# Kernel optimization log

Measured on AMD Instinct MI355X. Metric: run time of the kernel, lower is better.

The kernel has to match this reference:

```python
import jax, jax.numpy as jnp
import numpy as np

EPS = 1e-5

def _conv3x3(x, w, stride=1):
    # x: [N,C,H,W], w: [O,C,3,3]
    return jax.lax.conv_general_dilated(
        x, w, window_strides=(stride, stride), padding=((1, 1), (1, 1)),
        dimension_numbers=('NCHW', 'OIHW', 'NCHW'))

def _bn(x, gamma, beta, mean, var):
    # eval-mode BatchNorm2d over channel axis 1
    inv = jax.lax.rsqrt(var + EPS)
    return (x - mean[None, :, None, None]) * (gamma * inv)[None, :, None, None] + beta[None, :, None, None]

def setup_inputs() -> dict:
    key = jax.random.key(0)
    ks = jax.random.split(key, 8)
    C = 128
    x = jax.random.normal(ks[0], (64, C, 56, 56), dtype=jnp.float32)
    w1 = jax.random.normal(ks[1], (C, C, 3, 3), dtype=jnp.float32) * 0.05
    w2 = jax.random.normal(ks[2], (C, C, 3, 3), dtype=jnp.float32) * 0.05
    gamma1 = jnp.ones((C,), jnp.float32)
    beta1 = jnp.zeros((C,), jnp.float32)
    mean1 = jax.random.normal(ks[3], (C,), dtype=jnp.float32) * 0.1
    var1 = jax.random.uniform(ks[4], (C,), minval=0.5, maxval=1.5, dtype=jnp.float32)
    gamma2 = jnp.ones((C,), jnp.float32)
    beta2 = jnp.zeros((C,), jnp.float32)
    mean2 = jax.random.normal(ks[5], (C,), dtype=jnp.float32) * 0.1
    var2 = jax.random.uniform(ks[6], (C,), minval=0.5, maxval=1.5, dtype=jnp.float32)
    return {"x": x, "w1": w1, "w2": w2,
            "gamma1": gamma1, "beta1": beta1, "mean1": mean1, "var1": var1,
            "gamma2": gamma2, "beta2": beta2, "mean2": mean2, "var2": var2}

def reference(x, w1, w2, gamma1, beta1, mean1, var1, gamma2, beta2, mean2, var2):
    # BasicBlock forward. The voting loop over global dict d is a no-op (d = {}).
    residual = x
    out = _conv3x3(x, w1, stride=1)
    out = jax.nn.relu(_bn(out, gamma1, beta1, mean1, var1))
    out = _conv3x3(out, w2, stride=1)
    out = _bn(out, gamma2, beta2, mean2, var2)
    return jax.nn.relu(out + residual)
```

## Files before the change

### kernel.cpp

```cpp
#include <hip/hip_runtime.h>
#include <cstdint>

typedef __attribute__((ext_vector_type(8))) short bf16x8;
typedef __attribute__((ext_vector_type(4))) float f32x4;
typedef unsigned short u16;
typedef uint32_t u32;

#define HW56 56
#define HWSQ 3136
#define MTOT 200704
#define CCH 128
#define BM 128
#define NSTEP 18
#define NBLK (MTOT / BM)
#define NB_PER_XCD (NBLK / 8)

__device__ __forceinline__ u16 f2bf(float f) {
  u32 u = __builtin_bit_cast(u32, f);
  u = (u + 0x7fffu + ((u >> 16) & 1u)) >> 16;
  return (u16)u;
}
__device__ __forceinline__ float bf2f(u16 h) {
  return __builtin_bit_cast(float, (u32)h << 16);
}
__device__ __forceinline__ void gload16(const void* g, void* l) {
  __builtin_amdgcn_global_load_lds((const __attribute__((address_space(1))) void*)g,
                                   (__attribute__((address_space(3))) void*)l, 16, 0, 0);
}

__global__ __launch_bounds__(256) void pack_x_kernel(const float* __restrict__ x,
                                                     u16* __restrict__ xb) {
  __shared__ u16 t[128 * 65];
  const int tid = threadIdx.x;
  const int lane = tid & 63, wv = tid >> 6;
  const int p0 = blockIdx.x * 64;
  const int n = p0 / HWSQ, hw0 = p0 % HWSQ;
  const float* src = x + (size_t)(n * CCH) * HWSQ + hw0;
#pragma unroll
  for (int k = 0; k < 32; ++k) {
    const int c = wv * 32 + k;
    t[c * 65 + lane] = f2bf(src[(size_t)c * HWSQ + lane]);
  }
  __syncthreads();
  u16* dst = xb + (size_t)p0 * CCH;
#pragma unroll
  for (int it = 0; it < 4; ++it) {
    const int u = it * 256 + tid;
    const int pos = u >> 4, ch0 = (u & 15) * 8;
    u32 vv[4];
#pragma unroll
    for (int q = 0; q < 4; ++q) {
      const u16 a = t[(ch0 + 2 * q) * 65 + pos];
      const u16 b = t[(ch0 + 2 * q + 1) * 65 + pos];
      vv[q] = (u32)a | ((u32)b << 16);
    }
    uint4 v; v.x = vv[0]; v.y = vv[1]; v.z = vv[2]; v.w = vv[3];
    *(uint4*)(dst + (size_t)pos * CCH + ch0) = v;
  }
}

__global__ __launch_bounds__(256) void pack_w_kernel(
    const float* __restrict__ w1, const float* __restrict__ w2,
    const float* __restrict__ g1, const float* __restrict__ be1,
    const float* __restrict__ mu1, const float* __restrict__ va1,
    const float* __restrict__ g2, const float* __restrict__ be2,
    const float* __restrict__ mu2, const float* __restrict__ va2,
    u16* __restrict__ w1p, u16* __restrict__ w2p,
    float* __restrict__ b1, float* __restrict__ b2, float* __restrict__ zp) {
  const int idx = blockIdx.x * 256 + threadIdx.x;
  if (idx < 2 * 147456) {
    const int which = idx >= 147456;
    const int j = which ? idx - 147456 : idx;
    const int t = j >> 14;
    const int oc = (j >> 7) & 127;
    const int ic = j & 127;
    const float* w = which ? w2 : w1;
    const float* gg = which ? g2 : g1;
    const float* va = which ? va2 : va1;
    const float s = gg[oc] * rsqrtf(va[oc] + 1e-5f);
    const float val = w[(size_t)(oc * 128 + ic) * 9 + t] * s;
    (which ? w2p : w1p)[j] = f2bf(val);
  }
  if (blockIdx.x == 0) {
    const int t = threadIdx.x;
    if (t < 128) {
      const float s1 = g1[t] * rsqrtf(va1[t] + 1e-5f);
      b1[t] = be1[t] - mu1[t] * s1;
      const float s2 = g2[t] * rsqrtf(va2[t] + 1e-5f);
      b2[t] = be2[t] - mu2[t] * s2;
    }
    if (t < 64) zp[t] = 0.f;
  }
}

template <int PASS>
__global__ __launch_bounds__(256, 2) void conv_mfma(
    const u16* __restrict__ src, const u16* __restrict__ wp,
    const float* __restrict__ bias, const u16* __restrict__ resid,
    u16* __restrict__ outb, float* __restrict__ outf,
    const char* __restrict__ zp) {
  __shared__ __align__(1024) char lds[65536];
  const int tid = threadIdx.x;
  const int wave = tid >> 6, lane = tid & 63;
  const int bid = blockIdx.x;
  const int swz = (bid & 7) * NB_PER_XCD + (bid >> 3);
  const int m0 = swz * BM;
  const int wm = wave >> 1, wn = wave & 1;

  const int g = lane & 7;
  int ah[4], aw[4];
  long long aoff[4], boff[4];
#pragma unroll
  for (int i = 0; i < 4; ++i) {
    const int r = wave * 32 + i * 8 + (lane >> 3);
    const int pos = m0 + r;
    const int hw = pos % HWSQ;
    ah[i] = hw / HW56;
    aw[i] = hw % HW56;
    const int gsw = g ^ (r & 7);
    aoff[i] = (long long)pos * 256 + gsw * 16;
    boff[i] = (long long)r * 256 + gsw * 16;
  }
  const char* srcb = (const char*)src;
  const char* wpb = (const char*)wp;

  auto stage = [&](int buf, int s) {
    const int t = s >> 1, kh = s & 1;
    const int dyo = t / 3 - 1, dxo = t % 3 - 1;
    const long long adelta = (long long)(dyo * HW56 + dxo) * 256 + kh * 128;
    const long long bdelta = (long long)t * 32768 + kh * 128;
    char* ldsA = lds + buf * 16384;
    char* ldsB = lds + 32768 + buf * 16384;
#pragma unroll
    for (int i = 0; i < 4; ++i) {
      const int hh = ah[i] + dyo, ww = aw[i] + dxo;
      const bool valid = ((unsigned)hh < 56u) & ((unsigned)ww < 56u);
      const char* ap = valid ? (srcb + aoff[i] + adelta) : zp;
      gload16(ap, ldsA + (wave * 32 + i * 8) * 128);
      gload16(wpb + boff[i] + bdelta, ldsB + (wave * 32 + i * 8) * 128);
    }
  };

  f32x4 acc[4][4];
#pragma unroll
  for (int m = 0; m < 4; ++m)
#pragma unroll
    for (int n = 0; n < 4; ++n) {
      f32x4 z = {0.f, 0.f, 0.f, 0.f};
      acc[m][n] = z;
    }

  auto compute = [&](int buf) {
    const char* ldsA = lds + buf * 16384;
    const char* ldsB = lds + 32768 + buf * 16384;
    bf16x8 a[4][2], b[4][2];
#pragma unroll
    for (int m = 0; m < 4; ++m) {
      const int row = wm * 64 + m * 16 + (lane & 15);
      const char* rp = ldsA + row * 128;
      const int sw = row & 7;
#pragma unroll
      for (int ks = 0; ks < 2; ++ks) {
        const int gg = ks * 4 + (lane >> 4);
        a[m][ks] = *(const bf16x8*)(rp + ((gg ^ sw) << 4));
      }
    }
#pragma unroll
    for (int n = 0; n < 4; ++n) {
      const int row = wn * 64 + n * 16 + (lane & 15);
      const char* rp = ldsB + row * 128;
      const int sw = row & 7;
#pragma unroll
      for (int ks = 0; ks < 2; ++ks) {
        const int gg = ks * 4 + (lane >> 4);
        b[n][ks] = *(const bf16x8*)(rp + ((gg ^ sw) << 4));
      }
    }
#pragma unroll
    for (int ks = 0; ks < 2; ++ks)
#pragma unroll
      for (int m = 0; m < 4; ++m)
#pragma unroll
        for (int n = 0; n < 4; ++n)
          acc[m][n] = __builtin_amdgcn_mfma_f32_16x16x32_bf16(a[m][ks], b[n][ks],
                                                              acc[m][n], 0, 0, 0);
  };

  stage(0, 0);
  __syncthreads();
#pragma unroll
  for (int s = 0; s < NSTEP; ++s) {
    const int cur = s & 1;
    if (s + 1 < NSTEP) stage(cur ^ 1, s + 1);
    compute(cur);
    __syncthreads();
  }

  if (PASS == 1) {
#pragma unroll
    for (int nf = 0; nf < 4; ++nf) {
      const int oc = wn * 64 + nf * 16 + (lane & 15);
      const float bb = bias[oc];
#pragma unroll
      for (int m = 0; m < 4; ++m) {
        const int pbase = m0 + wm * 64 + m * 16 + (lane >> 4) * 4;
#pragma unroll
        for (int r = 0; r < 4; ++r) {
          float v = acc[m][nf][r] + bb;
          v = fmaxf(v, 0.f);
          outb[(size_t)(pbase + r) * CCH + oc] = f2bf(v);
        }
      }
    }
  } else {
    float* tl = (float*)(lds + wave * 4352);
    const int posr = m0 + wm * 64 + lane;
    const int nimg = posr / HWSQ, hwr = posr % HWSQ;
#pragma unroll
    for (int nf = 0; nf < 4; ++nf) {
      const int oc = wn * 64 + nf * 16 + (lane & 15);
      const float bb = bias[oc];
#pragma unroll
      for (int m = 0; m < 4; ++m) {
#pragma unroll
        for (int r = 0; r < 4; ++r) {
          const int row = m * 16 + (lane >> 4) * 4 + r;
          const int pos = m0 + wm * 64 + row;
          const float rv = bf2f(resid[(size_t)pos * CCH + oc]);
          float v = acc[m][nf][r] + bb + rv;
          tl[row * 17 + (lane & 15)] = fmaxf(v, 0.f);
        }
      }
#pragma unroll
      for (int oci = 0; oci < 16; ++oci) {
        const float v = tl[lane * 17 + oci];
        const int oc2 = wn * 64 + nf * 16 + oci;
        outf[(size_t)(nimg * CCH + oc2) * HWSQ + hwr] = v;
      }
    }
  }
}

extern "C" void kernel_launch(void* const* d_in, const int* in_sizes, int n_in,
                              void* d_out, int out_size, void* d_ws, size_t ws_size,
                              hipStream_t stream) {
  const float* x = (const float*)d_in[0];
  const float* w1 = (const float*)d_in[1];
  const float* w2 = (const float*)d_in[2];
  const float* g1 = (const float*)d_in[3];
  const float* be1 = (const float*)d_in[4];
  const float* mu1 = (const float*)d_in[5];
  const float* va1 = (const float*)d_in[6];
  const float* g2 = (const float*)d_in[7];
  const float* be2 = (const float*)d_in[8];
  const float* mu2 = (const float*)d_in[9];
  const float* va2 = (const float*)d_in[10];

  char* ws = (char*)d_ws;
  u16* xb  = (u16*)(ws + 0);
  u16* o1b = (u16*)(ws + 51380224);
  u16* w1p = (u16*)(ws + 102760448);
  u16* w2p = (u16*)(ws + 103055360);
  float* b1 = (float*)(ws + 103350272);
  float* b2 = (float*)(ws + 103350784);
  float* zp = (float*)(ws + 103351296);

  pack_x_kernel<<<MTOT / 64, 256, 0, stream>>>(x, xb);
  pack_w_kernel<<<1152, 256, 0, stream>>>(w1, w2, g1, be1, mu1, va1,
                                          g2, be2, mu2, va2, w1p, w2p, b1, b2, zp);
  conv_mfma<1><<<NBLK, 256, 0, stream>>>(xb, w1p, b1, nullptr, o1b, nullptr,
                                         (const char*)zp);
  conv_mfma<2><<<NBLK, 256, 0, stream>>>(o1b, w2p, b2, xb, nullptr, (float*)d_out,
                                         (const char*)zp);
}
```

Baseline: 335.9 us.

## Load weight fragments directly from global into registers, halve LDS for occupancy

The B (weight) operand is no longer staged through LDS. Each wave now reads its MFMA weight fragments straight from global memory into registers every step, relying on L2/L1 caching of the small weight tensor. This halves LDS use to 32KB, and launch bounds move to 3 blocks per SM to raise occupancy. The trade-off is that every wave issues redundant global loads for B with a small per-lane footprint (16B at a 256B stride). These loads may stall the MFMAs, and the register pressure from the higher occupancy target could cause spills.

```diff
diff --git a/kernel.cpp b/kernel.cpp
--- a/kernel.cpp
+++ b/kernel.cpp
@@ -94,12 +94,12 @@
 }
 
 template <int PASS>
-__global__ __launch_bounds__(256, 2) void conv_mfma(
+__global__ __launch_bounds__(256, 3) void conv_mfma(
     const u16* __restrict__ src, const u16* __restrict__ wp,
     const float* __restrict__ bias, const u16* __restrict__ resid,
     u16* __restrict__ outb, float* __restrict__ outf,
     const char* __restrict__ zp) {
-  __shared__ __align__(1024) char lds[65536];
+  __shared__ __align__(1024) char lds[32768];
   const int tid = threadIdx.x;
   const int wave = tid >> 6, lane = tid & 63;
   const int bid = blockIdx.x;
@@ -109,7 +109,7 @@
 
   const int g = lane & 7;
   int ah[4], aw[4];
-  long long aoff[4], boff[4];
+  long long aoff[4];
 #pragma unroll
   for (int i = 0; i < 4; ++i) {
     const int r = wave * 32 + i * 8 + (lane >> 3);
@@ -119,25 +119,21 @@
     aw[i] = hw % HW56;
     const int gsw = g ^ (r & 7);
     aoff[i] = (long long)pos * 256 + gsw * 16;
-    boff[i] = (long long)r * 256 + gsw * 16;
   }
   const char* srcb = (const char*)src;
-  const char* wpb = (const char*)wp;
-
-  auto stage = [&](int buf, int s) {
+  const char* wbase = (const char*)wp + (wn * 64 + (lane & 15)) * 256 + (lane >> 4) * 16;
+
+  auto stageA = [&](int buf, int s) {
     const int t = s >> 1, kh = s & 1;
     const int dyo = t / 3 - 1, dxo = t % 3 - 1;
     const long long adelta = (long long)(dyo * HW56 + dxo) * 256 + kh * 128;
-    const long long bdelta = (long long)t * 32768 + kh * 128;
     char* ldsA = lds + buf * 16384;
-    char* ldsB = lds + 32768 + buf * 16384;
 #pragma unroll
     for (int i = 0; i < 4; ++i) {
       const int hh = ah[i] + dyo, ww = aw[i] + dxo;
       const bool valid = ((unsigned)hh < 56u) & ((unsigned)ww < 56u);
       const char* ap = valid ? (srcb + aoff[i] + adelta) : zp;
       gload16(ap, ldsA + (wave * 32 + i * 8) * 128);
-      gload16(wpb + boff[i] + bdelta, ldsB + (wave * 32 + i * 8) * 128);
     }
   };
 
@@ -150,49 +146,42 @@
       acc[m][n] = z;
     }
 
-  auto compute = [&](int buf) {
-    const char* ldsA = lds + buf * 16384;
-    const char* ldsB = lds + 32768 + buf * 16384;
-    bf16x8 a[4][2], b[4][2];
-#pragma unroll
-    for (int m = 0; m < 4; ++m) {
-      const int row = wm * 64 + m * 16 + (lane & 15);
-      const char* rp = ldsA + row * 128;
-      const int sw = row & 7;
-#pragma unroll
-      for (int ks = 0; ks < 2; ++ks) {
-        const int gg = ks * 4 + (lane >> 4);
-        a[m][ks] = *(const bf16x8*)(rp + ((gg ^ sw) << 4));
-      }
-    }
-#pragma unroll
-    for (int n = 0; n < 4; ++n) {
-      const int row = wn * 64 + n * 16 + (lane & 15);
-      const char* rp = ldsB + row * 128;
-      const int sw = row & 7;
-#pragma unroll
-      for (int ks = 0; ks < 2; ++ks) {
-        const int gg = ks * 4 + (lane >> 4);
-        b[n][ks] = *(const bf16x8*)(rp + ((gg ^ sw) << 4));
-      }
-    }
-#pragma unroll
-    for (int ks = 0; ks < 2; ++ks)
-#pragma unroll
-      for (int m = 0; m < 4; ++m)
-#pragma unroll
-        for (int n = 0; n < 4; ++n)
-          acc[m][n] = __builtin_amdgcn_mfma_f32_16x16x32_bf16(a[m][ks], b[n][ks],
-                                                              acc[m][n], 0, 0, 0);
-  };
-
-  stage(0, 0);
+  stageA(0, 0);
   __syncthreads();
 #pragma unroll
   for (int s = 0; s < NSTEP; ++s) {
     const int cur = s & 1;
-    if (s + 1 < NSTEP) stage(cur ^ 1, s + 1);
-    compute(cur);
+    const int t = s >> 1, kh = s & 1;
+    bf16x8 b[4][2];
+#pragma unroll
+    for (int n = 0; n < 4; ++n)
+#pragma unroll
+      for (int ks = 0; ks < 2; ++ks)
+        b[n][ks] = *(const bf16x8*)(wbase + t * 32768 + kh * 128 + n * 4096 + ks * 64);
+    if (s + 1 < NSTEP) stageA(cur ^ 1, s + 1);
+    {
+      const char* ldsA = lds + cur * 16384;
+      bf16x8 a[4][2];
+#pragma unroll
+      for (int m = 0; m < 4; ++m) {
+        const int row = wm * 64 + m * 16 + (lane & 15);
+        const char* rp = ldsA + row * 128;
+        const int sw = row & 7;
+#pragma unroll
+        for (int ks = 0; ks < 2; ++ks) {
+          const int gg = ks * 4 + (lane >> 4);
+          a[m][ks] = *(const bf16x8*)(rp + ((gg ^ sw) << 4));
+        }
+      }
+#pragma unroll
+      for (int ks = 0; ks < 2; ++ks)
+#pragma unroll
+        for (int m = 0; m < 4; ++m)
+#pragma unroll
+          for (int n = 0; n < 4; ++n)
+            acc[m][n] = __builtin_amdgcn_mfma_f32_16x16x32_bf16(a[m][ks], b[n][ks],
+                                                                acc[m][n], 0, 0, 0);
+    }
     __syncthreads();
   }
 
```

Result: slower. 501.2 us (+49.2%).

## Add halo-padded NHWC layout and row-tile conv kernel with LDS-resident input

Applied to the files above, without the earlier changes.

Adds a zero-padded activation layout (58 rows × 64 cols per image) so each block of 512 threads loads a 6-row input halo into LDS once and reuses it across all nine 3x3 taps. Only the weights are double-buffered per step, and the per-tap bounds checks and zero-pointer gathers go away. The cost is extra padded columns computed as wasted MFMA work (64 vs 56), larger LDS use per block, and a workspace-size check that falls back to the old path when the workspace is too small.

```diff
diff --git a/kernel.cpp b/kernel.cpp
--- a/kernel.cpp
+++ b/kernel.cpp
@@ -10,10 +10,7 @@
 #define HWSQ 3136
 #define MTOT 200704
 #define CCH 128
-#define BM 128
 #define NSTEP 18
-#define NBLK (MTOT / BM)
-#define NB_PER_XCD (NBLK / 8)
 
 __device__ __forceinline__ u16 f2bf(float f) {
   u32 u = __builtin_bit_cast(u32, f);
@@ -28,34 +25,37 @@
                                    (__attribute__((address_space(3))) void*)l, 16, 0, 0);
 }
 
-__global__ __launch_bounds__(256) void pack_x_kernel(const float* __restrict__ x,
-                                                     u16* __restrict__ xb) {
-  __shared__ u16 t[128 * 65];
+
+__global__ __launch_bounds__(256) void pack_x_pad(const float* __restrict__ x,
+                                                  u16* __restrict__ xb2) {
+  __shared__ u16 t[56 * 130];
   const int tid = threadIdx.x;
   const int lane = tid & 63, wv = tid >> 6;
-  const int p0 = blockIdx.x * 64;
-  const int n = p0 / HWSQ, hw0 = p0 % HWSQ;
-  const float* src = x + (size_t)(n * CCH) * HWSQ + hw0;
-#pragma unroll
-  for (int k = 0; k < 32; ++k) {
-    const int c = wv * 32 + k;
-    t[c * 65 + lane] = f2bf(src[(size_t)c * HWSQ + lane]);
+  const int b = blockIdx.x;
+  const int n = b / 56, h = b % 56;
+  const float* src = x + ((size_t)n * CCH) * HWSQ + h * HW56;
+  if (lane < 56) {
+#pragma unroll
+    for (int k = 0; k < 32; ++k) {
+      const int c = wv * 32 + k;
+      t[lane * 130 + c] = f2bf(src[(size_t)c * HWSQ + lane]);
+    }
   }
   __syncthreads();
-  u16* dst = xb + (size_t)p0 * CCH;
-#pragma unroll
-  for (int it = 0; it < 4; ++it) {
-    const int u = it * 256 + tid;
-    const int pos = u >> 4, ch0 = (u & 15) * 8;
+  u16* dst = xb2 + ((size_t)(n * 58 + h + 1) * 64) * CCH;
+  const int w = tid >> 2, c0 = (tid & 3) * 32;
+#pragma unroll
+  for (int v4 = 0; v4 < 4; ++v4) {
     u32 vv[4];
 #pragma unroll
-    for (int q = 0; q < 4; ++q) {
-      const u16 a = t[(ch0 + 2 * q) * 65 + pos];
-      const u16 b = t[(ch0 + 2 * q + 1) * 65 + pos];
-      vv[q] = (u32)a | ((u32)b << 16);
-    }
-    uint4 v; v.x = vv[0]; v.y = vv[1]; v.z = vv[2]; v.w = vv[3];
-    *(uint4*)(dst + (size_t)pos * CCH + ch0) = v;
+    for (int qq = 0; qq < 4; ++qq) {
+      const int c = c0 + v4 * 8 + qq * 2;
+      u16 a = 0, bb = 0;
+      if (w < 56) { a = t[w * 130 + c]; bb = t[w * 130 + c + 1]; }
+      vv[qq] = (u32)a | ((u32)bb << 16);
+    }
+    uint4 V; V.x = vv[0]; V.y = vv[1]; V.z = vv[2]; V.w = vv[3];
+    *(uint4*)(dst + (size_t)w * CCH + c0 + v4 * 8) = V;
   }
 }
 
@@ -66,7 +66,25 @@
     const float* __restrict__ g2, const float* __restrict__ be2,
     const float* __restrict__ mu2, const float* __restrict__ va2,
     u16* __restrict__ w1p, u16* __restrict__ w2p,
-    float* __restrict__ b1, float* __restrict__ b2, float* __restrict__ zp) {
+    float* __restrict__ b1, float* __restrict__ b2, float* __restrict__ zp,
+    u16* __restrict__ hz1, u16* __restrict__ hz2) {
+  if (blockIdx.x >= 1152) {
+    if (hz1) {
+      const uint4 z4 = {0u, 0u, 0u, 0u};
+      const int u = (blockIdx.x - 1152) * 256 + threadIdx.x;
+#pragma unroll
+      for (int k = 0; k < 2; ++k) {
+        const int v = u * 2 + k;
+        const int img = v >> 11;
+        const int rr = (v >> 10) & 1;
+        const int off = v & 1023;
+        const size_t rowbase = ((size_t)(img * 58 + (rr ? 57 : 0)) * 64) * CCH;
+        *(uint4*)(hz1 + rowbase + off * 8) = z4;
+        *(uint4*)(hz2 + rowbase + off * 8) = z4;
+      }
+    }
+    return;
+  }
   const int idx = blockIdx.x * 256 + threadIdx.x;
   if (idx < 2 * 147456) {
     const int which = idx >= 147456;
@@ -94,6 +112,168 @@
 }
 
 template <int PASS>
+__global__ __launch_bounds__(512, 2) void conv_halo(
+    const u16* __restrict__ src, const u16* __restrict__ wp,
+    const float* __restrict__ bias, const u16* __restrict__ resid,
+    u16* __restrict__ outb, float* __restrict__ outf) {
+  __shared__ __align__(1024) char lds[256 + 98304 + 512 + 32768];
+  char* const Abase = lds + 256;
+  char* const Bbase = lds + 256 + 98304 + 512;
+  const int tid = threadIdx.x;
+  const int wave = tid >> 6, lane = tid & 63;
+  const int wm = wave >> 1, wn = wave & 1;
+  const int l15 = lane & 15, q = lane >> 4;
+  const int bid = blockIdx.x;
+  const int swz = (bid & 7) * 112 + (bid >> 3);
+  const int n = swz / 14, rg = swz % 14, h0 = rg * 4;
+
+  if (tid < 16) { const uint4 z4 = {0u,0u,0u,0u}; *(uint4*)(lds + tid * 16) = z4; }
+
+  const char* Asrc = (const char*)src + ((size_t)(n * 58 + h0) * 64) * 256;
+  const u32 aswz = (((u32)tid >> 4) & 7) << 4;
+#pragma unroll
+  for (int rd = 0; rd < 12; ++rd) {
+    const u32 d = rd * 8192 + tid * 16;
+    gload16(Asrc + (d ^ aswz), Abase + d);
+  }
+
+  const u32 bswz = (((u32)tid >> 3) & 7) << 4;
+  auto stageB = [&](int buf, int s) {
+    const int t = s >> 1, kh = s & 1;
+    const char* base = (const char*)wp + t * 32768 + kh * 128;
+    char* ldsB = Bbase + buf * 16384;
+#pragma unroll
+    for (int i = 0; i < 2; ++i) {
+      const u32 d = i * 8192 + tid * 16;
+      const u32 srcoff = ((d & 0xFFFFFF80u) << 1) | ((d & 0x70u) ^ bswz);
+      gload16(base + srcoff, ldsB + d);
+    }
+  };
+
+  f32x4 acc[4][4];
+#pragma unroll
+  for (int m = 0; m < 4; ++m)
+#pragma unroll
+    for (int nf = 0; nf < 4; ++nf) {
+      f32x4 z = {0.f, 0.f, 0.f, 0.f};
+      acc[m][nf] = z;
+    }
+
+  stageB(0, 0);
+  __syncthreads();
+
+#pragma unroll
+  for (int s = 0; s < NSTEP; ++s) {
+    const int t = s >> 1, kh = s & 1;
+    const int dy = t / 3 - 1, dx = t % 3 - 1;
+    if (s + 1 < NSTEP) stageB((s + 1) & 1, s + 1);
+    const char* Bb = Bbase + (s & 1) * 16384;
+    bf16x8 bfr[4][2];
+#pragma unroll
+    for (int nf = 0; nf < 4; ++nf) {
+      const char* rp = Bb + (wn * 64 + nf * 16 + l15) * 128;
+#pragma unroll
+      for (int ks = 0; ks < 2; ++ks)
+        bfr[nf][ks] = *(const bf16x8*)(rp + (((ks * 4 + q) ^ (lane & 7)) << 4));
+    }
+    bf16x8 afr[4][2];
+#pragma unroll
+    for (int m = 0; m < 4; ++m) {
+      const int arow = (wm + 1 + dy) * 64 + m * 16 + l15 + dx;
+      const char* rp = Abase + arow * 256;
+      const int s3 = arow & 7;
+#pragma unroll
+      for (int ks = 0; ks < 2; ++ks)
+        afr[m][ks] = *(const bf16x8*)(rp + ((kh * 8 + ((ks * 4 + q) ^ s3)) << 4));
+    }
+#pragma unroll
+    for (int ks = 0; ks < 2; ++ks)
+#pragma unroll
+      for (int m = 0; m < 4; ++m)
+#pragma unroll
+        for (int nf = 0; nf < 4; ++nf)
+          acc[m][nf] = __builtin_amdgcn_mfma_f32_16x16x32_bf16(afr[m][ks], bfr[nf][ks],
+                                                               acc[m][nf], 0, 0, 0);
+    __syncthreads();
+  }
+
+  const int h = h0 + wm;
+  if (PASS == 1) {
+    u16* orow = outb + ((size_t)(n * 58 + h + 1) * 64) * CCH;
+#pragma unroll
+    for (int nf = 0; nf < 4; ++nf) {
+      const int oc = wn * 64 + nf * 16 + l15;
+      const float bb = bias[oc];
+#pragma unroll
+      for (int m = 0; m < 4; ++m)
+#pragma unroll
+        for (int r = 0; r < 4; ++r) {
+          const int w = m * 16 + q * 4 + r;
+          const float v = (w < 56) ? fmaxf(acc[m][nf][r] + bb, 0.f) : 0.f;
+          orow[(size_t)w * CCH + oc] = f2bf(v);
+        }
+    }
+  } else {
+    float* tl = (float*)(lds + wave * 4352);
+    const u16* rrow = resid + ((size_t)(n * 58 + h + 1) * 64) * CCH;
+#pragma unroll
+    for (int nf = 0; nf < 4; ++nf) {
+      const int oc = wn * 64 + nf * 16 + l15;
+      const float bb = bias[oc];
+#pragma unroll
+      for (int m = 0; m < 4; ++m)
+#pragma unroll
+        for (int r = 0; r < 4; ++r) {
+          const int w = m * 16 + q * 4 + r;
+          const float rv = bf2f(rrow[(size_t)w * CCH + oc]);
+          tl[w * 17 + l15] = fmaxf(acc[m][nf][r] + bb + rv, 0.f);
+        }
+#pragma unroll
+      for (int oci = 0; oci < 16; ++oci) {
+        const float v = tl[lane * 17 + oci];
+        if (lane < 56)
+          outf[((size_t)n * CCH + wn * 64 + nf * 16 + oci) * HWSQ + h * HW56 + lane] = v;
+      }
+    }
+  }
+}
+
+#define BM 128
+#define NBLK (MTOT / BM)
+#define NB_PER_XCD (NBLK / 8)
+
+__global__ __launch_bounds__(256) void pack_x_kernel(const float* __restrict__ x,
+                                                     u16* __restrict__ xb) {
+  __shared__ u16 t[128 * 65];
+  const int tid = threadIdx.x;
+  const int lane = tid & 63, wv = tid >> 6;
+  const int p0 = blockIdx.x * 64;
+  const int n = p0 / HWSQ, hw0 = p0 % HWSQ;
+  const float* src = x + (size_t)(n * CCH) * HWSQ + hw0;
+#pragma unroll
+  for (int k = 0; k < 32; ++k) {
+    const int c = wv * 32 + k;
+    t[c * 65 + lane] = f2bf(src[(size_t)c * HWSQ + lane]);
+  }
+  __syncthreads();
+  u16* dst = xb + (size_t)p0 * CCH;
+#pragma unroll
+  for (int it = 0; it < 4; ++it) {
+    const int u = it * 256 + tid;
+    const int pos = u >> 4, ch0 = (u & 15) * 8;
+    u32 vv[4];
+#pragma unroll
+    for (int qq = 0; qq < 4; ++qq) {
+      const u16 a = t[(ch0 + 2 * qq) * 65 + pos];
+      const u16 b = t[(ch0 + 2 * qq + 1) * 65 + pos];
+      vv[qq] = (u32)a | ((u32)b << 16);
+    }
+    uint4 v; v.x = vv[0]; v.y = vv[1]; v.z = vv[2]; v.w = vv[3];
+    *(uint4*)(dst + (size_t)pos * CCH + ch0) = v;
+  }
+}
+
+template <int PASS>
 __global__ __launch_bounds__(256, 2) void conv_mfma(
     const u16* __restrict__ src, const u16* __restrict__ wp,
     const float* __restrict__ bias, const u16* __restrict__ resid,
@@ -106,7 +286,6 @@
   const int swz = (bid & 7) * NB_PER_XCD + (bid >> 3);
   const int m0 = swz * BM;
   const int wm = wave >> 1, wn = wave & 1;
-
   const int g = lane & 7;
   int ah[4], aw[4];
   long long aoff[4], boff[4];
@@ -123,7 +302,6 @@
   }
   const char* srcb = (const char*)src;
   const char* wpb = (const char*)wp;
-
   auto stage = [&](int buf, int s) {
     const int t = s >> 1, kh = s & 1;
     const int dyo = t / 3 - 1, dxo = t % 3 - 1;
@@ -140,16 +318,14 @@
       gload16(wpb + boff[i] + bdelta, ldsB + (wave * 32 + i * 8) * 128);
     }
   };
-
   f32x4 acc[4][4];
 #pragma unroll
   for (int m = 0; m < 4; ++m)
 #pragma unroll
-    for (int n = 0; n < 4; ++n) {
+    for (int nf = 0; nf < 4; ++nf) {
       f32x4 z = {0.f, 0.f, 0.f, 0.f};
-      acc[m][n] = z;
-    }
-
+      acc[m][nf] = z;
+    }
   auto compute = [&](int buf) {
     const char* ldsA = lds + buf * 16384;
     const char* ldsB = lds + 32768 + buf * 16384;
@@ -166,14 +342,14 @@
       }
     }
 #pragma unroll
-    for (int n = 0; n < 4; ++n) {
-      const int row = wn * 64 + n * 16 + (lane & 15);
+    for (int nf = 0; nf < 4; ++nf) {
+      const int row = wn * 64 + nf * 16 + (lane & 15);
       const char* rp = ldsB + row * 128;
       const int sw = row & 7;
 #pragma unroll
       for (int ks = 0; ks < 2; ++ks) {
         const int gg = ks * 4 + (lane >> 4);
-        b[n][ks] = *(const bf16x8*)(rp + ((gg ^ sw) << 4));
+        b[nf][ks] = *(const bf16x8*)(rp + ((gg ^ sw) << 4));
       }
     }
 #pragma unroll
@@ -181,11 +357,10 @@
 #pragma unroll
       for (int m = 0; m < 4; ++m)
 #pragma unroll
-        for (int n = 0; n < 4; ++n)
-          acc[m][n] = __builtin_amdgcn_mfma_f32_16x16x32_bf16(a[m][ks], b[n][ks],
-                                                              acc[m][n], 0, 0, 0);
+        for (int nf = 0; nf < 4; ++nf)
+          acc[m][nf] = __builtin_amdgcn_mfma_f32_16x16x32_bf16(a[m][ks], b[nf][ks],
+                                                               acc[m][nf], 0, 0, 0);
   };
-
   stage(0, 0);
   __syncthreads();
 #pragma unroll
@@ -195,7 +370,6 @@
     compute(cur);
     __syncthreads();
   }
-
   if (PASS == 1) {
 #pragma unroll
     for (int nf = 0; nf < 4; ++nf) {
@@ -257,19 +431,39 @@
   const float* va2 = (const float*)d_in[10];
 
   char* ws = (char*)d_ws;
-  u16* xb  = (u16*)(ws + 0);
-  u16* o1b = (u16*)(ws + 51380224);
-  u16* w1p = (u16*)(ws + 102760448);
-  u16* w2p = (u16*)(ws + 103055360);
-  float* b1 = (float*)(ws + 103350272);
-  float* b2 = (float*)(ws + 103350784);
-  float* zp = (float*)(ws + 103351296);
-
-  pack_x_kernel<<<MTOT / 64, 256, 0, stream>>>(x, xb);
-  pack_w_kernel<<<1152, 256, 0, stream>>>(w1, w2, g1, be1, mu1, va1,
-                                          g2, be2, mu2, va2, w1p, w2p, b1, b2, zp);
-  conv_mfma<1><<<NBLK, 256, 0, stream>>>(xb, w1p, b1, nullptr, o1b, nullptr,
-                                         (const char*)zp);
-  conv_mfma<2><<<NBLK, 256, 0, stream>>>(o1b, w2p, b2, xb, nullptr, (float*)d_out,
-                                         (const char*)zp);
-}
+  const size_t PADSZ = (size_t)64 * 58 * 64 * 128 * 2;
+
+  if (ws_size >= 2 * PADSZ + 2 * 294912 + 2048) {
+    u16* xb2  = (u16*)(ws + 0);
+    u16* o1b2 = (u16*)(ws + PADSZ);
+    u16* w1p  = (u16*)(ws + 2 * PADSZ);
+    u16* w2p  = (u16*)(ws + 2 * PADSZ + 294912);
+    float* b1 = (float*)(ws + 2 * PADSZ + 2 * 294912);
+    float* b2 = (float*)(ws + 2 * PADSZ + 2 * 294912 + 512);
+    float* zp = (float*)(ws + 2 * PADSZ + 2 * 294912 + 1024);
+
+    pack_x_pad<<<64 * 56, 256, 0, stream>>>(x, xb2);
+    pack_w_kernel<<<1152 + 256, 256, 0, stream>>>(w1, w2, g1, be1, mu1, va1,
+                                                  g2, be2, mu2, va2, w1p, w2p,
+                                                  b1, b2, zp, xb2, o1b2);
+    conv_halo<1><<<896, 512, 0, stream>>>(xb2, w1p, b1, nullptr, o1b2, nullptr);
+    conv_halo<2><<<896, 512, 0, stream>>>(o1b2, w2p, b2, xb2, nullptr, (float*)d_out);
+  } else {
+    u16* xb  = (u16*)(ws + 0);
+    u16* o1b = (u16*)(ws + 51380224);
+    u16* w1p = (u16*)(ws + 102760448);
+    u16* w2p = (u16*)(ws + 103055360);
+    float* b1 = (float*)(ws + 103350272);
+    float* b2 = (float*)(ws + 103350784);
+    float* zp = (float*)(ws + 103351296);
+
+    pack_x_kernel<<<MTOT / 64, 256, 0, stream>>>(x, xb);
+    pack_w_kernel<<<1152, 256, 0, stream>>>(w1, w2, g1, be1, mu1, va1,
+                                            g2, be2, mu2, va2, w1p, w2p,
+                                            b1, b2, zp, nullptr, nullptr);
+    conv_mfma<1><<<NBLK, 256, 0, stream>>>(xb, w1p, b1, nullptr, o1b, nullptr,
+                                           (const char*)zp);
+    conv_mfma<2><<<NBLK, 256, 0, stream>>>(o1b, w2p, b2, xb, nullptr, (float*)d_out,
+                                           (const char*)zp);
+  }
+}
```

After: 359.0 us. 1.07x slower.

## Halve K-slice per pipeline stage to cut LDS and raise occupancy

Applied to the files above, without the earlier changes.

The per-stage K chunk drops from 64 to 32 channels, doubling the step count to 36 and halving the double-buffered LDS footprint to 32 KB. The staging layout, swizzle and fragment loads are rewritten for 64-byte rows, and launch bounds ask for 4 blocks per CU instead of 2. The aim is more resident waves to hide global-load latency, at the cost of twice as many barriers and less MFMA work between syncs. Tighter register limits could also cause spills with the 64-float accumulator.

```diff
diff --git a/kernel.cpp b/kernel.cpp
--- a/kernel.cpp
+++ b/kernel.cpp
@@ -11,7 +11,7 @@
 #define MTOT 200704
 #define CCH 128
 #define BM 128
-#define NSTEP 18
+#define NSTEP 36
 #define NBLK (MTOT / BM)
 #define NB_PER_XCD (NBLK / 8)
 
@@ -94,30 +94,31 @@
 }
 
 template <int PASS>
-__global__ __launch_bounds__(256, 2) void conv_mfma(
+__global__ __launch_bounds__(256, 4) void conv_mfma(
     const u16* __restrict__ src, const u16* __restrict__ wp,
     const float* __restrict__ bias, const u16* __restrict__ resid,
     u16* __restrict__ outb, float* __restrict__ outf,
     const char* __restrict__ zp) {
-  __shared__ __align__(1024) char lds[65536];
+  __shared__ __align__(1024) char lds[32768];
   const int tid = threadIdx.x;
   const int wave = tid >> 6, lane = tid & 63;
+  const int l15 = lane & 15, q = lane >> 4;
   const int bid = blockIdx.x;
   const int swz = (bid & 7) * NB_PER_XCD + (bid >> 3);
   const int m0 = swz * BM;
   const int wm = wave >> 1, wn = wave & 1;
 
-  const int g = lane & 7;
-  int ah[4], aw[4];
-  long long aoff[4], boff[4];
-#pragma unroll
-  for (int i = 0; i < 4; ++i) {
-    const int r = wave * 32 + i * 8 + (lane >> 3);
+  const int g = tid & 3;
+  int ah[2], aw[2];
+  long long aoff[2], boff[2];
+#pragma unroll
+  for (int i = 0; i < 2; ++i) {
+    const int r = i * 64 + (tid >> 2);
     const int pos = m0 + r;
     const int hw = pos % HWSQ;
     ah[i] = hw / HW56;
     aw[i] = hw % HW56;
-    const int gsw = g ^ (r & 7);
+    const int gsw = g ^ (r & 3);
     aoff[i] = (long long)pos * 256 + gsw * 16;
     boff[i] = (long long)r * 256 + gsw * 16;
   }
@@ -125,19 +126,19 @@
   const char* wpb = (const char*)wp;
 
   auto stage = [&](int buf, int s) {
-    const int t = s >> 1, kh = s & 1;
+    const int t = s >> 2, kh2 = s & 3;
     const int dyo = t / 3 - 1, dxo = t % 3 - 1;
-    const long long adelta = (long long)(dyo * HW56 + dxo) * 256 + kh * 128;
-    const long long bdelta = (long long)t * 32768 + kh * 128;
-    char* ldsA = lds + buf * 16384;
-    char* ldsB = lds + 32768 + buf * 16384;
-#pragma unroll
-    for (int i = 0; i < 4; ++i) {
+    const long long adelta = (long long)(dyo * HW56 + dxo) * 256 + kh2 * 64;
+    const long long bdelta = (long long)t * 32768 + kh2 * 64;
+    char* ldsA = lds + buf * 8192;
+    char* ldsB = lds + 16384 + buf * 8192;
+#pragma unroll
+    for (int i = 0; i < 2; ++i) {
       const int hh = ah[i] + dyo, ww = aw[i] + dxo;
       const bool valid = ((unsigned)hh < 56u) & ((unsigned)ww < 56u);
       const char* ap = valid ? (srcb + aoff[i] + adelta) : zp;
-      gload16(ap, ldsA + (wave * 32 + i * 8) * 128);
-      gload16(wpb + boff[i] + bdelta, ldsB + (wave * 32 + i * 8) * 128);
+      gload16(ap, ldsA + i * 4096 + wave * 1024);
+      gload16(wpb + boff[i] + bdelta, ldsB + i * 4096 + wave * 1024);
     }
   };
 
@@ -151,39 +152,25 @@
     }
 
   auto compute = [&](int buf) {
-    const char* ldsA = lds + buf * 16384;
-    const char* ldsB = lds + 32768 + buf * 16384;
-    bf16x8 a[4][2], b[4][2];
+    const char* ldsA = lds + buf * 8192;
+    const char* ldsB = lds + 16384 + buf * 8192;
+    bf16x8 a[4], b[4];
 #pragma unroll
     for (int m = 0; m < 4; ++m) {
-      const int row = wm * 64 + m * 16 + (lane & 15);
-      const char* rp = ldsA + row * 128;
-      const int sw = row & 7;
-#pragma unroll
-      for (int ks = 0; ks < 2; ++ks) {
-        const int gg = ks * 4 + (lane >> 4);
-        a[m][ks] = *(const bf16x8*)(rp + ((gg ^ sw) << 4));
-      }
+      const int row = wm * 64 + m * 16 + l15;
+      a[m] = *(const bf16x8*)(ldsA + row * 64 + ((q ^ (row & 3)) << 4));
     }
 #pragma unroll
     for (int n = 0; n < 4; ++n) {
-      const int row = wn * 64 + n * 16 + (lane & 15);
-      const char* rp = ldsB + row * 128;
-      const int sw = row & 7;
-#pragma unroll
-      for (int ks = 0; ks < 2; ++ks) {
-        const int gg = ks * 4 + (lane >> 4);
-        b[n][ks] = *(const bf16x8*)(rp + ((gg ^ sw) << 4));
-      }
-    }
-#pragma unroll
-    for (int ks = 0; ks < 2; ++ks)
-#pragma unroll
-      for (int m = 0; m < 4; ++m)
-#pragma unroll
-        for (int n = 0; n < 4; ++n)
-          acc[m][n] = __builtin_amdgcn_mfma_f32_16x16x32_bf16(a[m][ks], b[n][ks],
-                                                              acc[m][n], 0, 0, 0);
+      const int row = wn * 64 + n * 16 + l15;
+      b[n] = *(const bf16x8*)(ldsB + row * 64 + ((q ^ (row & 3)) << 4));
+    }
+#pragma unroll
+    for (int m = 0; m < 4; ++m)
+#pragma unroll
+      for (int n = 0; n < 4; ++n)
+        acc[m][n] = __builtin_amdgcn_mfma_f32_16x16x32_bf16(a[m], b[n],
+                                                            acc[m][n], 0, 0, 0);
   };
 
   stage(0, 0);
@@ -199,11 +186,11 @@
   if (PASS == 1) {
 #pragma unroll
     for (int nf = 0; nf < 4; ++nf) {
-      const int oc = wn * 64 + nf * 16 + (lane & 15);
+      const int oc = wn * 64 + nf * 16 + l15;
       const float bb = bias[oc];
 #pragma unroll
       for (int m = 0; m < 4; ++m) {
-        const int pbase = m0 + wm * 64 + m * 16 + (lane >> 4) * 4;
+        const int pbase = m0 + wm * 64 + m * 16 + q * 4;
 #pragma unroll
         for (int r = 0; r < 4; ++r) {
           float v = acc[m][nf][r] + bb;
@@ -218,17 +205,17 @@
     const int nimg = posr / HWSQ, hwr = posr % HWSQ;
 #pragma unroll
     for (int nf = 0; nf < 4; ++nf) {
-      const int oc = wn * 64 + nf * 16 + (lane & 15);
+      const int oc = wn * 64 + nf * 16 + l15;
       const float bb = bias[oc];
 #pragma unroll
       for (int m = 0; m < 4; ++m) {
 #pragma unroll
         for (int r = 0; r < 4; ++r) {
-          const int row = m * 16 + (lane >> 4) * 4 + r;
+          const int row = m * 16 + q * 4 + r;
           const int pos = m0 + wm * 64 + row;
           const float rv = bf2f(resid[(size_t)pos * CCH + oc]);
           float v = acc[m][nf][r] + bb + rv;
-          tl[row * 17 + (lane & 15)] = fmaxf(v, 0.f);
+          tl[row * 17 + l15] = fmaxf(v, 0.f);
         }
       }
 #pragma unroll
```

New measurement: 355.5 us. 1.06x slower.
